# Kernel tuning notes

Hardware: AMD Instinct MI355X
Metric: run time of the kernel (lower is better)

## Reference

```python
import jax, jax.numpy as jnp
import numpy as np

HEADS = 8
DIM_HEAD = 64
SCALE = DIM_HEAD ** -0.5


def setup_inputs() -> dict:
    key = jax.random.key(0)
    ks = jax.random.split(key, 6)
    B, N, M = 4, 4096, 1024
    QD, CD, ID = 320, 768, 512
    s = lambda d: (1.0 / np.sqrt(d)).astype(np.float32)
    return {
        "x": jax.random.normal(ks[0], (B, N, QD), dtype=jnp.float32),
        "context": jax.random.normal(ks[1], (B, M, CD), dtype=jnp.float32),
        "Wq": jax.random.normal(ks[2], (QD, ID), dtype=jnp.float32) * s(QD),
        "Wk": jax.random.normal(ks[3], (CD, ID), dtype=jnp.float32) * s(CD),
        "Wv": jax.random.normal(ks[4], (CD, ID), dtype=jnp.float32) * s(CD),
        "Wo": jax.random.normal(ks[5], (ID, QD), dtype=jnp.float32) * s(ID),
        "bo": jnp.zeros((QD,), dtype=jnp.float32),
    }


def reference(x, context, Wq, Wk, Wv, Wo, bo):
    B, N, _ = x.shape
    M = context.shape[1]
    # projections
    q = (x @ Wq).reshape(B, N, HEADS, DIM_HEAD)        # b n h d
    k = (context @ Wk).reshape(B, M, HEADS, DIM_HEAD)  # b m h d
    v = (context @ Wv).reshape(B, M, HEADS, DIM_HEAD)
    # scaled dot-product attention per head
    scores = jnp.einsum("bnhd,bmhd->bhnm", q, k) * SCALE
    attn = jax.nn.softmax(scores, axis=-1)
    out = jnp.einsum("bhnm,bmhd->bnhd", attn, v).reshape(B, N, HEADS * DIM_HEAD)
    # output projection (dropout p=0.0 is identity)
    return out @ Wo + bo
```

## Files before the change

### kernel.cpp

```cpp
#include <hip/hip_runtime.h>
#include <cmath>

constexpr int BATCH  = 4;
constexpr int SEQ_N  = 4096;
constexpr int SEQ_M  = 1024;
constexpr int QD     = 320;
constexpr int CD     = 768;
constexpr int ID     = 512;
constexpr float QFOLD = 0.125f * 1.44269504f;
constexpr float EK2F  = -8.0f * 1.44269504f;

typedef __bf16 bf16x8 __attribute__((ext_vector_type(8)));
typedef __bf16 bf16x4 __attribute__((ext_vector_type(4)));
typedef __bf16 bf16x2 __attribute__((ext_vector_type(2)));
typedef float  f32x4  __attribute__((ext_vector_type(4)));

__device__ __forceinline__ void gload_lds16(const __bf16* g, __bf16* l) {
    __builtin_amdgcn_global_load_lds(
        (const __attribute__((address_space(1))) void*)g,
        (__attribute__((address_space(3))) void*)l, 16, 0, 0);
}

__device__ __forceinline__ float fast_exp2(float x) {
#if __has_builtin(__builtin_amdgcn_exp2f)
    return __builtin_amdgcn_exp2f(x);
#else
    return exp2f(x);
#endif
}

__global__ __launch_bounds__(256)
void cvt_all(const float* __restrict__ x, const float* __restrict__ ctx,
             const float* __restrict__ Wq, const float* __restrict__ Wk,
             const float* __restrict__ Wv, const float* __restrict__ Wo,
             __bf16* __restrict__ xb, __bf16* __restrict__ ctxb,
             __bf16* __restrict__ WqT, __bf16* __restrict__ WkT,
             __bf16* __restrict__ WvT, __bf16* __restrict__ WoT) {
    __shared__ float tile[32][33];
    int bid = blockIdx.x;
    if (bid < 4096) {
        constexpr int NX8 = SEQ_N * BATCH * QD / 8;
        int i = bid * 256 + threadIdx.x;
        const float* s; __bf16* d; int j;
        if (i < NX8) { s = x; d = xb; j = i; }
        else         { s = ctx; d = ctxb; j = i - NX8; }
        const float4* sp = reinterpret_cast<const float4*>(s) + (size_t)j * 2;
        float4 a = sp[0], b = sp[1];
        bf16x8 o = { (__bf16)a.x, (__bf16)a.y, (__bf16)a.z, (__bf16)a.w,
                     (__bf16)b.x, (__bf16)b.y, (__bf16)b.z, (__bf16)b.w };
        reinterpret_cast<bf16x8*>(d)[j] = o;
        return;
    }
    int wb = bid - 4096;
    const float* W; __bf16* WT; int K, N, tid; float scl = 1.0f;
    if (wb < 160)      { W = Wq; WT = WqT; K = 320; N = 512; tid = wb; scl = QFOLD; }
    else if (wb < 544) { W = Wk; WT = WkT; K = 768; N = 512; tid = wb - 160; }
    else if (wb < 928) { W = Wv; WT = WvT; K = 768; N = 512; tid = wb - 544; }
    else               { W = Wo; WT = WoT; K = 512; N = 320; tid = wb - 928; }
    int kt = K / 32;
    int k0 = (tid % kt) * 32, n0 = (tid / kt) * 32;
    int tc = threadIdx.x & 31, tr = threadIdx.x >> 5;
#pragma unroll
    for (int p = 0; p < 4; ++p)
        tile[p * 8 + tr][tc] = W[(size_t)(k0 + p * 8 + tr) * N + n0 + tc];
    __syncthreads();
#pragma unroll
    for (int p = 0; p < 4; ++p)
        WT[(size_t)(n0 + p * 8 + tr) * K + k0 + tc] = (__bf16)(tile[tc][p * 8 + tr] * scl);
}

__global__ __launch_bounds__(256)
void gemm_kv(const __bf16* __restrict__ A, const __bf16* __restrict__ BT,
             __bf16* __restrict__ Kb, __bf16* __restrict__ Vt, int M, int K) {
    __shared__ __attribute__((aligned(16))) __bf16 sA[2][128][64];
    __shared__ __attribute__((aligned(16))) __bf16 sB[2][64][64];

    const int t = threadIdx.x;
    const int wave = t >> 6, lane = t & 63;
    const int q = lane >> 4, c = lane & 15;
    const int wm = wave >> 1, wn = wave & 1;
    const int row0 = blockIdx.x * 128, col0 = blockIdx.y * 64;
    const int srow = lane >> 3, sch = lane & 7;
    const int fch = sch ^ srow;

    auto stage = [&](int buf, int k0) {
#pragma unroll
        for (int i = 0; i < 4; ++i) {
            int r = wave * 32 + i * 8;
            gload_lds16(A + (size_t)(row0 + r + srow) * K + k0 + fch * 8,
                        &sA[buf][r][0] + lane * 8);
        }
#pragma unroll
        for (int i = 0; i < 2; ++i) {
            int r = wave * 16 + i * 8;
            gload_lds16(BT + (size_t)(col0 + r + srow) * K + k0 + fch * 8,
                        &sB[buf][r][0] + lane * 8);
        }
    };

    f32x4 acc[4][2] = {};
    stage(0, 0);
    const int iters = K >> 6;
    for (int it = 0; it < iters; ++it) {
        const int p = it & 1;
        __syncthreads();
        if (it + 1 < iters) stage(p ^ 1, (it + 1) * 64);
#pragma unroll
        for (int ks = 0; ks < 2; ++ks) {
            const int so = ((ks * 4 + q) ^ (c & 7)) * 8;
            bf16x8 am[4], bn[2];
#pragma unroll
            for (int i = 0; i < 4; ++i)
                am[i] = *reinterpret_cast<const bf16x8*>(&sA[p][wm * 64 + i * 16 + c][0] + so);
#pragma unroll
            for (int j = 0; j < 2; ++j)
                bn[j] = *reinterpret_cast<const bf16x8*>(&sB[p][wn * 32 + j * 16 + c][0] + so);
#pragma unroll
            for (int i = 0; i < 4; ++i)
#pragma unroll
                for (int j = 0; j < 2; ++j)
                    acc[i][j] = __builtin_amdgcn_mfma_f32_16x16x32_bf16(bn[j], am[i], acc[i][j], 0, 0, 0);
        }
    }

    if (blockIdx.y < 8) {
#pragma unroll
        for (int i = 0; i < 4; ++i)
#pragma unroll
            for (int j = 0; j < 2; ++j) {
                int mrow = row0 + wm * 64 + i * 16 + c;
                int ncol = col0 + wn * 32 + j * 16 + q * 4;
                bf16x4 v = { (__bf16)acc[i][j][0], (__bf16)acc[i][j][1],
                             (__bf16)acc[i][j][2], (__bf16)acc[i][j][3] };
                *reinterpret_cast<bf16x4*>(&Kb[(size_t)mrow * 512 + ncol]) = v;
            }
    } else {
        __bf16* ldsT = (__bf16*)sA;
        __syncthreads();
#pragma unroll
        for (int i = 0; i < 4; ++i)
#pragma unroll
            for (int j = 0; j < 2; ++j) {
                int ml = wm * 64 + i * 16 + c;
                int dl = wn * 32 + j * 16 + q * 4;
#pragma unroll
                for (int r = 0; r < 4; ++r)
                    ldsT[(dl + r) * 136 + ml] = (__bf16)acc[i][j][r];
            }
        __syncthreads();
        int b = row0 >> 10, m0 = row0 & 1023;
        int h = (col0 - 512) >> 6;
        int d = t >> 2, ch = t & 3;
        __bf16* dst = Vt + (((size_t)((b * 8 + h) * 64 + d)) << 10) + m0 + ch * 32;
        const __bf16* src = &ldsT[d * 136 + ch * 32];
#pragma unroll
        for (int u = 0; u < 4; ++u)
            *reinterpret_cast<bf16x8*>(dst + u * 8) = *reinterpret_cast<const bf16x8*>(src + u * 8);
    }
}

__global__ __launch_bounds__(256, 2)
void flash_attn(const __bf16* __restrict__ xb, const __bf16* __restrict__ WqT,
                const __bf16* __restrict__ Kb, const __bf16* __restrict__ Vt,
                __bf16* __restrict__ AO) {
    __shared__ __attribute__((aligned(16))) __bf16 smem[20480];

    const int t = threadIdx.x;
    const int wave = t >> 6, lane = t & 63;
    const int q = lane >> 4, c = lane & 15;
    const int bh = blockIdx.y;
    const int b = bh >> 3, h = bh & 7;
    const int n0 = blockIdx.x * 256;
    const int srow = lane >> 3, sch = lane & 7;
    const int fch = sch ^ srow;

    f32x4 accQ[4][4] = {};
    {
        __bf16* sX = smem;
        __bf16* sW = smem + 16384;
        for (int k0 = 0; k0 < QD; k0 += 64) {
            __syncthreads();
#pragma unroll
            for (int i = 0; i < 8; ++i) {
                int r = wave * 64 + i * 8;
                gload_lds16(xb + (size_t)(b * SEQ_N + n0 + r + srow) * QD + k0 + fch * 8,
                            sX + r * 64 + lane * 8);
            }
#pragma unroll
            for (int i = 0; i < 2; ++i) {
                int r = wave * 16 + i * 8;
                gload_lds16(WqT + (size_t)(h * 64 + r + srow) * QD + k0 + fch * 8,
                            sW + r * 64 + lane * 8);
            }
            __syncthreads();
#pragma unroll
            for (int ks = 0; ks < 2; ++ks) {
                const int so = ((ks * 4 + q) ^ (c & 7)) * 8;
                bf16x8 aw[4], bx[4];
#pragma unroll
                for (int dt = 0; dt < 4; ++dt)
                    aw[dt] = *reinterpret_cast<const bf16x8*>(sW + (dt * 16 + c) * 64 + so);
#pragma unroll
                for (int qt = 0; qt < 4; ++qt)
                    bx[qt] = *reinterpret_cast<const bf16x8*>(sX + (wave * 64 + qt * 16 + c) * 64 + so);
#pragma unroll
                for (int dt = 0; dt < 4; ++dt)
#pragma unroll
                    for (int qt = 0; qt < 4; ++qt)
                        accQ[dt][qt] = __builtin_amdgcn_mfma_f32_16x16x32_bf16(aw[dt], bx[qt], accQ[dt][qt], 0, 0, 0);
            }
        }
    }
    __syncthreads();

    __bf16* sQw = smem + wave * 4608;
#pragma unroll
    for (int dt = 0; dt < 4; ++dt)
#pragma unroll
        for (int qt = 0; qt < 4; ++qt) {
            bf16x2 w0 = { (__bf16)accQ[dt][qt][0], (__bf16)accQ[dt][qt][1] };
            bf16x2 w1 = { (__bf16)accQ[dt][qt][2], (__bf16)accQ[dt][qt][3] };
            __bf16* pr = sQw + (qt * 16 + c) * 72 + dt * 16 + q * 4;
            *reinterpret_cast<bf16x2*>(pr)     = w0;
            *reinterpret_cast<bf16x2*>(pr + 2) = w1;
        }
    bf16x8 aq[4][2];
#pragma unroll
    for (int qt = 0; qt < 4; ++qt)
#pragma unroll
        for (int ks = 0; ks < 2; ++ks)
            aq[qt][ks] = *reinterpret_cast<const bf16x8*>(sQw + (qt * 16 + c) * 72 + ks * 32 + q * 8);
    __syncthreads();

    auto stageKV = [&](int buf, int m0) {
        __bf16* sK = smem + buf * 8192;
        __bf16* sV = smem + buf * 8192 + 4096;
#pragma unroll
        for (int i = 0; i < 2; ++i) {
            int r = wave * 16 + i * 8;
            int rho = r + srow;
            int kl = (rho & 32) | (((rho & 15) >> 2) << 3)
                   | (rho & 3) | (((rho >> 4) & 1) << 2);
            gload_lds16(Kb + (size_t)(b * SEQ_M + m0 + kl) * ID + h * 64 + fch * 8,
                        sK + r * 64 + lane * 8);
            gload_lds16(Vt + (((size_t)((b * 8 + h) * 64 + rho)) << 10) + m0 + fch * 8,
                        sV + r * 64 + lane * 8);
        }
    };

    const f32x4 ekc = { EK2F, EK2F, EK2F, EK2F };
    const bf16x8 ONES = { (__bf16)1.0f, (__bf16)1.0f, (__bf16)1.0f, (__bf16)1.0f,
                          (__bf16)1.0f, (__bf16)1.0f, (__bf16)1.0f, (__bf16)1.0f };
    f32x4 accO[4][4] = {};
    f32x4 accL[4] = {};

    stageKV(0, 0);
    constexpr int TILES = SEQ_M / 64;
    for (int mt = 0; mt < TILES; ++mt) {
        const int p = mt & 1;
        __syncthreads();
        if (mt + 1 < TILES) stageKV(p ^ 1, (mt + 1) * 64);
        const __bf16* sK = smem + p * 8192;
        const __bf16* sV = smem + p * 8192 + 4096;

        f32x4 s[4][4];
        __builtin_amdgcn_s_setprio(1);
#pragma unroll
        for (int ks = 0; ks < 2; ++ks) {
            const int so = ((ks * 4 + q) ^ (c & 7)) * 8;
#pragma unroll
            for (int ct = 0; ct < 4; ++ct) {
                bf16x8 ak = *reinterpret_cast<const bf16x8*>(sK + (ct * 16 + c) * 64 + so);
#pragma unroll
                for (int qt = 0; qt < 4; ++qt)
                    s[qt][ct] = (ks == 0)
                        ? __builtin_amdgcn_mfma_f32_16x16x32_bf16(ak, aq[qt][0], ekc, 0, 0, 0)
                        : __builtin_amdgcn_mfma_f32_16x16x32_bf16(ak, aq[qt][1], s[qt][ct], 0, 0, 0);
            }
        }
        __builtin_amdgcn_s_setprio(0);

        bf16x8 bp[4][2];
#pragma unroll
        for (int qt = 0; qt < 4; ++qt) {
            float pp[16];
#pragma unroll
            for (int ct = 0; ct < 4; ++ct)
#pragma unroll
                for (int r = 0; r < 4; ++r)
                    pp[ct * 4 + r] = fast_exp2(s[qt][ct][r]);
#pragma unroll
            for (int g = 0; g < 2; ++g)
                bp[qt][g] = bf16x8{ (__bf16)pp[g * 8 + 0], (__bf16)pp[g * 8 + 1],
                                    (__bf16)pp[g * 8 + 2], (__bf16)pp[g * 8 + 3],
                                    (__bf16)pp[g * 8 + 4], (__bf16)pp[g * 8 + 5],
                                    (__bf16)pp[g * 8 + 6], (__bf16)pp[g * 8 + 7] };
        }

        __builtin_amdgcn_s_setprio(1);
#pragma unroll
        for (int ks = 0; ks < 2; ++ks) {
            const int so = ((ks * 4 + q) ^ (c & 7)) * 8;
#pragma unroll
            for (int qt = 0; qt < 4; ++qt)
                accL[qt] = __builtin_amdgcn_mfma_f32_16x16x32_bf16(ONES, bp[qt][ks], accL[qt], 0, 0, 0);
#pragma unroll
            for (int nt = 0; nt < 4; ++nt) {
                bf16x8 av = *reinterpret_cast<const bf16x8*>(sV + (nt * 16 + c) * 64 + so);
#pragma unroll
                for (int qt = 0; qt < 4; ++qt)
                    accO[qt][nt] = __builtin_amdgcn_mfma_f32_16x16x32_bf16(av, bp[qt][ks], accO[qt][nt], 0, 0, 0);
            }
        }
        __builtin_amdgcn_s_setprio(0);
    }

#pragma unroll
    for (int qt = 0; qt < 4; ++qt) {
        float inv = 1.0f / accL[qt][0];
        size_t rowb = (size_t)(b * SEQ_N + n0 + wave * 64 + qt * 16 + c) * ID + h * 64;
#pragma unroll
        for (int nt = 0; nt < 4; ++nt) {
            bf16x4 v = { (__bf16)(accO[qt][nt][0] * inv), (__bf16)(accO[qt][nt][1] * inv),
                         (__bf16)(accO[qt][nt][2] * inv), (__bf16)(accO[qt][nt][3] * inv) };
            *reinterpret_cast<bf16x4*>(&AO[rowb + nt * 16 + q * 4]) = v;
        }
    }
}

__global__ __launch_bounds__(256)
void gemm_out(const __bf16* __restrict__ A, const __bf16* __restrict__ BT,
              const float* __restrict__ bias, float* __restrict__ C,
              int M, int N, int K) {
    __shared__ __attribute__((aligned(16))) __bf16 sA[2][128][64];
    __shared__ __attribute__((aligned(16))) __bf16 sB[2][64][64];

    const int t = threadIdx.x;
    const int wave = t >> 6, lane = t & 63;
    const int q = lane >> 4, c = lane & 15;
    const int wm = wave >> 1, wn = wave & 1;
    const int row0 = blockIdx.x * 128, col0 = blockIdx.y * 64;
    const int srow = lane >> 3, sch = lane & 7;
    const int fch = sch ^ srow;

    auto stage = [&](int buf, int k0) {
#pragma unroll
        for (int i = 0; i < 4; ++i) {
            int r = wave * 32 + i * 8;
            gload_lds16(A + (size_t)(row0 + r + srow) * K + k0 + fch * 8,
                        &sA[buf][r][0] + lane * 8);
        }
#pragma unroll
        for (int i = 0; i < 2; ++i) {
            int r = wave * 16 + i * 8;
            gload_lds16(BT + (size_t)(col0 + r + srow) * K + k0 + fch * 8,
                        &sB[buf][r][0] + lane * 8);
        }
    };

    f32x4 acc[4][2] = {};
    stage(0, 0);
    const int iters = K >> 6;
    for (int it = 0; it < iters; ++it) {
        const int p = it & 1;
        __syncthreads();
        if (it + 1 < iters) stage(p ^ 1, (it + 1) * 64);
#pragma unroll
        for (int ks = 0; ks < 2; ++ks) {
            const int so = ((ks * 4 + q) ^ (c & 7)) * 8;
            bf16x8 am[4], bn[2];
#pragma unroll
            for (int i = 0; i < 4; ++i)
                am[i] = *reinterpret_cast<const bf16x8*>(&sA[p][wm * 64 + i * 16 + c][0] + so);
#pragma unroll
            for (int j = 0; j < 2; ++j)
                bn[j] = *reinterpret_cast<const bf16x8*>(&sB[p][wn * 32 + j * 16 + c][0] + so);
#pragma unroll
            for (int i = 0; i < 4; ++i)
#pragma unroll
                for (int j = 0; j < 2; ++j)
                    acc[i][j] = __builtin_amdgcn_mfma_f32_16x16x32_bf16(bn[j], am[i], acc[i][j], 0, 0, 0);
        }
    }

#pragma unroll
    for (int i = 0; i < 4; ++i)
#pragma unroll
        for (int j = 0; j < 2; ++j) {
            int mrow = row0 + wm * 64 + i * 16 + c;
            int ncol = col0 + wn * 32 + j * 16 + q * 4;
            float4 v = { acc[i][j][0] + bias[ncol + 0],
                         acc[i][j][1] + bias[ncol + 1],
                         acc[i][j][2] + bias[ncol + 2],
                         acc[i][j][3] + bias[ncol + 3] };
            *reinterpret_cast<float4*>(&C[(size_t)mrow * N + ncol]) = v;
        }
}

extern "C" void kernel_launch(void* const* d_in, const int* in_sizes, int n_in,
                              void* d_out, int out_size, void* d_ws, size_t ws_size,
                              hipStream_t stream) {
    const float* x   = (const float*)d_in[0];
    const float* ctx = (const float*)d_in[1];
    const float* Wq  = (const float*)d_in[2];
    const float* Wk  = (const float*)d_in[3];
    const float* Wv  = (const float*)d_in[4];
    const float* Wo  = (const float*)d_in[5];
    const float* bo  = (const float*)d_in[6];
    float* out = (float*)d_out;

    char* ws = (char*)d_ws;
    __bf16* xb   = (__bf16*)(ws + 0);
    __bf16* ctxb = (__bf16*)(ws + 10485760);
    __bf16* AO   = (__bf16*)(ws + 16777216);
    __bf16* Kb   = (__bf16*)(ws + 33554432);
    __bf16* Vt   = (__bf16*)(ws + 37748736);
    __bf16* WqT  = (__bf16*)(ws + 41943040);
    __bf16* WkT  = (__bf16*)(ws + 42270720);
    __bf16* WvT  = (__bf16*)(ws + 43057152);
    __bf16* WoT  = (__bf16*)(ws + 43843584);

    const int MX = BATCH * SEQ_N;
    const int MC = BATCH * SEQ_M;
    dim3 blk(256);

    cvt_all<<<dim3(5184), blk, 0, stream>>>(x, ctx, Wq, Wk, Wv, Wo,
                                            xb, ctxb, WqT, WkT, WvT, WoT);

    gemm_kv<<<dim3(MC / 128, 16), blk, 0, stream>>>(ctxb, WkT, Kb, Vt, MC, CD);

    flash_attn<<<dim3(SEQ_N / 256, 32), blk, 0, stream>>>(xb, WqT, Kb, Vt, AO);

    gemm_out<<<dim3(MX / 128, QD / 64), blk, 0, stream>>>(AO, WoT, bo, out, MX, QD, ID);
}
```

Measured before the change: 155.5 us.

## Overlap x conversion with KV GEMM and software-pipeline two KV tiles per iteration

The fp32-to-bf16 conversion of x moves out of the pre-pass kernel and into extra blocks of the KV projection GEMM launch (now a 1D grid), so it runs alongside the GEMM instead of before it. In flash attention, each loop iteration now processes two 64-row K/V tiles and interleaves the second tile's QK MFMAs with the first tile's exp2 and PV, so MFMA and transcendental work can overlap. The s_setprio hints are dropped. LDS use grows from 40KB to 64KB per block for four tile buffers, which may limit the two-blocks-per-CU occupancy target, and the extra live score/probability registers raise register pressure.

```diff
diff --git a/kernel.cpp b/kernel.cpp
--- a/kernel.cpp
+++ b/kernel.cpp
@@ -30,33 +30,29 @@
 }
 
 __global__ __launch_bounds__(256)
-void cvt_all(const float* __restrict__ x, const float* __restrict__ ctx,
+void cvt_pre(const float* __restrict__ ctx,
              const float* __restrict__ Wq, const float* __restrict__ Wk,
              const float* __restrict__ Wv, const float* __restrict__ Wo,
-             __bf16* __restrict__ xb, __bf16* __restrict__ ctxb,
+             __bf16* __restrict__ ctxb,
              __bf16* __restrict__ WqT, __bf16* __restrict__ WkT,
              __bf16* __restrict__ WvT, __bf16* __restrict__ WoT) {
     __shared__ float tile[32][33];
     int bid = blockIdx.x;
-    if (bid < 4096) {
-        constexpr int NX8 = SEQ_N * BATCH * QD / 8;
-        int i = bid * 256 + threadIdx.x;
-        const float* s; __bf16* d; int j;
-        if (i < NX8) { s = x; d = xb; j = i; }
-        else         { s = ctx; d = ctxb; j = i - NX8; }
-        const float4* sp = reinterpret_cast<const float4*>(s) + (size_t)j * 2;
+    if (bid < 1536) {
+        int j = bid * 256 + threadIdx.x;
+        const float4* sp = reinterpret_cast<const float4*>(ctx) + (size_t)j * 2;
         float4 a = sp[0], b = sp[1];
         bf16x8 o = { (__bf16)a.x, (__bf16)a.y, (__bf16)a.z, (__bf16)a.w,
                      (__bf16)b.x, (__bf16)b.y, (__bf16)b.z, (__bf16)b.w };
-        reinterpret_cast<bf16x8*>(d)[j] = o;
+        reinterpret_cast<bf16x8*>(ctxb)[j] = o;
         return;
     }
-    int wb = bid - 4096;
+    int wb = bid - 1536;
     const float* W; __bf16* WT; int K, N, tid; float scl = 1.0f;
-    if (wb < 160)      { W = Wq; WT = WqT; K = 320; N = 512; tid = wb; scl = QFOLD; }
-    else if (wb < 544) { W = Wk; WT = WkT; K = 768; N = 512; tid = wb - 160; }
-    else if (wb < 928) { W = Wv; WT = WvT; K = 768; N = 512; tid = wb - 544; }
-    else               { W = Wo; WT = WoT; K = 512; N = 320; tid = wb - 928; }
+    if (wb < 384)       { W = Wk; WT = WkT; K = 768; N = 512; tid = wb; }
+    else if (wb < 768)  { W = Wv; WT = WvT; K = 768; N = 512; tid = wb - 384; }
+    else if (wb < 928)  { W = Wq; WT = WqT; K = 320; N = 512; tid = wb - 768; scl = QFOLD; }
+    else                { W = Wo; WT = WoT; K = 512; N = 320; tid = wb - 928; }
     int kt = K / 32;
     int k0 = (tid % kt) * 32, n0 = (tid / kt) * 32;
     int tc = threadIdx.x & 31, tr = threadIdx.x >> 5;
@@ -71,15 +67,28 @@
 
 __global__ __launch_bounds__(256)
 void gemm_kv(const __bf16* __restrict__ A, const __bf16* __restrict__ BT,
-             __bf16* __restrict__ Kb, __bf16* __restrict__ Vt, int M, int K) {
+             const float* __restrict__ x, __bf16* __restrict__ Kb,
+             __bf16* __restrict__ Vt, __bf16* __restrict__ xb, int K) {
     __shared__ __attribute__((aligned(16))) __bf16 sA[2][128][64];
     __shared__ __attribute__((aligned(16))) __bf16 sB[2][64][64];
+
+    int bid = blockIdx.x;
+    if (bid >= 512) {
+        int j = (bid - 512) * 256 + threadIdx.x;
+        const float4* sp = reinterpret_cast<const float4*>(x) + (size_t)j * 2;
+        float4 a = sp[0], b = sp[1];
+        bf16x8 o = { (__bf16)a.x, (__bf16)a.y, (__bf16)a.z, (__bf16)a.w,
+                     (__bf16)b.x, (__bf16)b.y, (__bf16)b.z, (__bf16)b.w };
+        reinterpret_cast<bf16x8*>(xb)[j] = o;
+        return;
+    }
 
     const int t = threadIdx.x;
     const int wave = t >> 6, lane = t & 63;
     const int q = lane >> 4, c = lane & 15;
     const int wm = wave >> 1, wn = wave & 1;
-    const int row0 = blockIdx.x * 128, col0 = blockIdx.y * 64;
+    const int by = bid >> 5;
+    const int row0 = (bid & 31) * 128, col0 = by * 64;
     const int srow = lane >> 3, sch = lane & 7;
     const int fch = sch ^ srow;
 
@@ -123,7 +132,7 @@
         }
     }
 
-    if (blockIdx.y < 8) {
+    if (by < 8) {
 #pragma unroll
         for (int i = 0; i < 4; ++i)
 #pragma unroll
@@ -163,7 +172,7 @@
 void flash_attn(const __bf16* __restrict__ xb, const __bf16* __restrict__ WqT,
                 const __bf16* __restrict__ Kb, const __bf16* __restrict__ Vt,
                 __bf16* __restrict__ AO) {
-    __shared__ __attribute__((aligned(16))) __bf16 smem[20480];
+    __shared__ __attribute__((aligned(16))) __bf16 smem[32768];
 
     const int t = threadIdx.x;
     const int wave = t >> 6, lane = t & 63;
@@ -232,9 +241,9 @@
             aq[qt][ks] = *reinterpret_cast<const bf16x8*>(sQw + (qt * 16 + c) * 72 + ks * 32 + q * 8);
     __syncthreads();
 
-    auto stageKV = [&](int buf, int m0) {
-        __bf16* sK = smem + buf * 8192;
-        __bf16* sV = smem + buf * 8192 + 4096;
+    auto stageT = [&](int ts, int m0) {
+        __bf16* sK = smem + ts * 8192;
+        __bf16* sV = smem + ts * 8192 + 4096;
 #pragma unroll
         for (int i = 0; i < 2; ++i) {
             int r = wave * 16 + i * 8;
@@ -254,17 +263,7 @@
     f32x4 accO[4][4] = {};
     f32x4 accL[4] = {};
 
-    stageKV(0, 0);
-    constexpr int TILES = SEQ_M / 64;
-    for (int mt = 0; mt < TILES; ++mt) {
-        const int p = mt & 1;
-        __syncthreads();
-        if (mt + 1 < TILES) stageKV(p ^ 1, (mt + 1) * 64);
-        const __bf16* sK = smem + p * 8192;
-        const __bf16* sV = smem + p * 8192 + 4096;
-
-        f32x4 s[4][4];
-        __builtin_amdgcn_s_setprio(1);
+    auto QK = [&](const __bf16* sK, f32x4 (&sarr)[4][4]) {
 #pragma unroll
         for (int ks = 0; ks < 2; ++ks) {
             const int so = ((ks * 4 + q) ^ (c & 7)) * 8;
@@ -273,14 +272,13 @@
                 bf16x8 ak = *reinterpret_cast<const bf16x8*>(sK + (ct * 16 + c) * 64 + so);
 #pragma unroll
                 for (int qt = 0; qt < 4; ++qt)
-                    s[qt][ct] = (ks == 0)
+                    sarr[qt][ct] = (ks == 0)
                         ? __builtin_amdgcn_mfma_f32_16x16x32_bf16(ak, aq[qt][0], ekc, 0, 0, 0)
-                        : __builtin_amdgcn_mfma_f32_16x16x32_bf16(ak, aq[qt][1], s[qt][ct], 0, 0, 0);
-            }
-        }
-        __builtin_amdgcn_s_setprio(0);
-
-        bf16x8 bp[4][2];
+                        : __builtin_amdgcn_mfma_f32_16x16x32_bf16(ak, aq[qt][1], sarr[qt][ct], 0, 0, 0);
+            }
+        }
+    };
+    auto EXP2P = [&](const f32x4 (&sarr)[4][4], bf16x8 (&bp)[4][2]) {
 #pragma unroll
         for (int qt = 0; qt < 4; ++qt) {
             float pp[16];
@@ -288,7 +286,7 @@
             for (int ct = 0; ct < 4; ++ct)
 #pragma unroll
                 for (int r = 0; r < 4; ++r)
-                    pp[ct * 4 + r] = fast_exp2(s[qt][ct][r]);
+                    pp[ct * 4 + r] = fast_exp2(sarr[qt][ct][r]);
 #pragma unroll
             for (int g = 0; g < 2; ++g)
                 bp[qt][g] = bf16x8{ (__bf16)pp[g * 8 + 0], (__bf16)pp[g * 8 + 1],
@@ -296,8 +294,8 @@
                                     (__bf16)pp[g * 8 + 4], (__bf16)pp[g * 8 + 5],
                                     (__bf16)pp[g * 8 + 6], (__bf16)pp[g * 8 + 7] };
         }
-
-        __builtin_amdgcn_s_setprio(1);
+    };
+    auto PV = [&](const __bf16* sV, const bf16x8 (&bp)[4][2]) {
 #pragma unroll
         for (int ks = 0; ks < 2; ++ks) {
             const int so = ((ks * 4 + q) ^ (c & 7)) * 8;
@@ -312,7 +310,31 @@
                     accO[qt][nt] = __builtin_amdgcn_mfma_f32_16x16x32_bf16(av, bp[qt][ks], accO[qt][nt], 0, 0, 0);
             }
         }
-        __builtin_amdgcn_s_setprio(0);
+    };
+
+    stageT(0, 0);
+    stageT(1, 64);
+    constexpr int ITERS = SEQ_M / 128;
+    for (int it = 0; it < ITERS; ++it) {
+        const int p = it & 1;
+        __syncthreads();
+        if (it + 1 < ITERS) {
+            stageT((p ^ 1) * 2,     (2 * it + 2) * 64);
+            stageT((p ^ 1) * 2 + 1, (2 * it + 3) * 64);
+        }
+        const __bf16* sKA = smem + (2 * p) * 8192;
+        const __bf16* sVA = sKA + 4096;
+        const __bf16* sKB = smem + (2 * p + 1) * 8192;
+        const __bf16* sVB = sKB + 4096;
+
+        f32x4 sA_[4][4]; bf16x8 bpA[4][2];
+        QK(sKA, sA_);
+        EXP2P(sA_, bpA);
+        f32x4 sB_[4][4]; bf16x8 bpB[4][2];
+        QK(sKB, sB_);
+        PV(sVA, bpA);
+        EXP2P(sB_, bpB);
+        PV(sVB, bpB);
     }
 
 #pragma unroll
@@ -421,13 +443,12 @@
     __bf16* WoT  = (__bf16*)(ws + 43843584);
 
     const int MX = BATCH * SEQ_N;
-    const int MC = BATCH * SEQ_M;
     dim3 blk(256);
 
-    cvt_all<<<dim3(5184), blk, 0, stream>>>(x, ctx, Wq, Wk, Wv, Wo,
-                                            xb, ctxb, WqT, WkT, WvT, WoT);
-
-    gemm_kv<<<dim3(MC / 128, 16), blk, 0, stream>>>(ctxb, WkT, Kb, Vt, MC, CD);
+    cvt_pre<<<dim3(2624), blk, 0, stream>>>(ctx, Wq, Wk, Wv, Wo,
+                                            ctxb, WqT, WkT, WvT, WoT);
+
+    gemm_kv<<<dim3(3072), blk, 0, stream>>>(ctxb, WkT, x, Kb, Vt, xb, CD);
 
     flash_attn<<<dim3(SEQ_N / 256, 32), blk, 0, stream>>>(xb, WqT, Kb, Vt, AO);
 
```

Result: slower. 170.9 us (+9.9%).

## Stagger wave groups so half the waves run PV while others run QK

Applied to the files above, without the earlier changes.

The flash-attention loop now splits the four waves into two groups. One group runs QK, exp and PV on the current tile. The other group defers PV of the previous tile to the start of the next iteration, so matrix-core work and exp work from different waves interleave. The K/V LDS ring grows from two to four slots so the deferred group can still read the previous V tile. This raises LDS use to 64KB per block, which may limit occupancy at two blocks per CU, and it removes the setprio hints.

```diff
diff --git a/kernel.cpp b/kernel.cpp
--- a/kernel.cpp
+++ b/kernel.cpp
@@ -163,7 +163,7 @@
 void flash_attn(const __bf16* __restrict__ xb, const __bf16* __restrict__ WqT,
                 const __bf16* __restrict__ Kb, const __bf16* __restrict__ Vt,
                 __bf16* __restrict__ AO) {
-    __shared__ __attribute__((aligned(16))) __bf16 smem[20480];
+    __shared__ __attribute__((aligned(16))) __bf16 smem[32768];
 
     const int t = threadIdx.x;
     const int wave = t >> 6, lane = t & 63;
@@ -232,9 +232,9 @@
             aq[qt][ks] = *reinterpret_cast<const bf16x8*>(sQw + (qt * 16 + c) * 72 + ks * 32 + q * 8);
     __syncthreads();
 
-    auto stageKV = [&](int buf, int m0) {
-        __bf16* sK = smem + buf * 8192;
-        __bf16* sV = smem + buf * 8192 + 4096;
+    auto stageKV = [&](int slot, int m0) {
+        __bf16* sK = smem + slot * 8192;
+        __bf16* sV = smem + slot * 8192 + 4096;
 #pragma unroll
         for (int i = 0; i < 2; ++i) {
             int r = wave * 16 + i * 8;
@@ -254,17 +254,7 @@
     f32x4 accO[4][4] = {};
     f32x4 accL[4] = {};
 
-    stageKV(0, 0);
-    constexpr int TILES = SEQ_M / 64;
-    for (int mt = 0; mt < TILES; ++mt) {
-        const int p = mt & 1;
-        __syncthreads();
-        if (mt + 1 < TILES) stageKV(p ^ 1, (mt + 1) * 64);
-        const __bf16* sK = smem + p * 8192;
-        const __bf16* sV = smem + p * 8192 + 4096;
-
-        f32x4 s[4][4];
-        __builtin_amdgcn_s_setprio(1);
+    auto QK = [&](const __bf16* sK, f32x4 (&sarr)[4][4]) {
 #pragma unroll
         for (int ks = 0; ks < 2; ++ks) {
             const int so = ((ks * 4 + q) ^ (c & 7)) * 8;
@@ -273,14 +263,13 @@
                 bf16x8 ak = *reinterpret_cast<const bf16x8*>(sK + (ct * 16 + c) * 64 + so);
 #pragma unroll
                 for (int qt = 0; qt < 4; ++qt)
-                    s[qt][ct] = (ks == 0)
+                    sarr[qt][ct] = (ks == 0)
                         ? __builtin_amdgcn_mfma_f32_16x16x32_bf16(ak, aq[qt][0], ekc, 0, 0, 0)
-                        : __builtin_amdgcn_mfma_f32_16x16x32_bf16(ak, aq[qt][1], s[qt][ct], 0, 0, 0);
-            }
-        }
-        __builtin_amdgcn_s_setprio(0);
-
-        bf16x8 bp[4][2];
+                        : __builtin_amdgcn_mfma_f32_16x16x32_bf16(ak, aq[qt][1], sarr[qt][ct], 0, 0, 0);
+            }
+        }
+    };
+    auto EXP2P = [&](const f32x4 (&sarr)[4][4], bf16x8 (&bp)[4][2]) {
 #pragma unroll
         for (int qt = 0; qt < 4; ++qt) {
             float pp[16];
@@ -288,7 +277,7 @@
             for (int ct = 0; ct < 4; ++ct)
 #pragma unroll
                 for (int r = 0; r < 4; ++r)
-                    pp[ct * 4 + r] = fast_exp2(s[qt][ct][r]);
+                    pp[ct * 4 + r] = fast_exp2(sarr[qt][ct][r]);
 #pragma unroll
             for (int g = 0; g < 2; ++g)
                 bp[qt][g] = bf16x8{ (__bf16)pp[g * 8 + 0], (__bf16)pp[g * 8 + 1],
@@ -296,8 +285,8 @@
                                     (__bf16)pp[g * 8 + 4], (__bf16)pp[g * 8 + 5],
                                     (__bf16)pp[g * 8 + 6], (__bf16)pp[g * 8 + 7] };
         }
-
-        __builtin_amdgcn_s_setprio(1);
+    };
+    auto PV = [&](const __bf16* sV, const bf16x8 (&bp)[4][2]) {
 #pragma unroll
         for (int ks = 0; ks < 2; ++ks) {
             const int so = ((ks * 4 + q) ^ (c & 7)) * 8;
@@ -312,8 +301,31 @@
                     accO[qt][nt] = __builtin_amdgcn_mfma_f32_16x16x32_bf16(av, bp[qt][ks], accO[qt][nt], 0, 0, 0);
             }
         }
-        __builtin_amdgcn_s_setprio(0);
-    }
+    };
+
+    stageKV(0, 0);
+    f32x4 s[4][4];
+    bf16x8 bp[4][2];
+    const bool gA = (wave < 2);
+    constexpr int TILES = SEQ_M / 64;
+    for (int mt = 0; mt < TILES; ++mt) {
+        __syncthreads();
+        if (mt + 1 < TILES) stageKV((mt + 1) & 3, (mt + 1) * 64);
+        const __bf16* sK  = smem + (mt & 3) * 8192;
+        const __bf16* sV  = sK + 4096;
+        const __bf16* sVp = smem + ((mt - 1) & 3) * 8192 + 4096;
+
+        if (gA) {
+            QK(sK, s);
+            EXP2P(s, bp);
+            PV(sV, bp);
+        } else {
+            if (mt > 0) PV(sVp, bp);
+            QK(sK, s);
+            EXP2P(s, bp);
+        }
+    }
+    if (!gA) PV(smem + ((TILES - 1) & 3) * 8192 + 4096, bp);
 
 #pragma unroll
     for (int qt = 0; qt < 4; ++qt) {
```

After: 157.6 us. No clear change (+1.4%).

## Fuse fp32-to-bf16 conversion of x into attention Q projection, VALU row sums

Applied to the files above, without the earlier changes.

Removes the separate conversion pass of x to bf16. The attention kernel now loads fp32 x directly from global memory and converts it to bf16 in registers before writing to LDS, which saves a full write and re-read of the xb buffer. The softmax denominator is now accumulated with VALU adds and finished with cross-lane shuffles instead of extra MFMAs against a ones vector. The setprio hints are also dropped. In exchange, each x tile is now loaded 8 times (once per head block), reading fp32 instead of bf16 and going through registers instead of direct-to-LDS loads.

```diff
diff --git a/kernel.cpp b/kernel.cpp
--- a/kernel.cpp
+++ b/kernel.cpp
@@ -30,33 +30,29 @@
 }
 
 __global__ __launch_bounds__(256)
-void cvt_all(const float* __restrict__ x, const float* __restrict__ ctx,
+void cvt_pre(const float* __restrict__ ctx,
              const float* __restrict__ Wq, const float* __restrict__ Wk,
              const float* __restrict__ Wv, const float* __restrict__ Wo,
-             __bf16* __restrict__ xb, __bf16* __restrict__ ctxb,
+             __bf16* __restrict__ ctxb,
              __bf16* __restrict__ WqT, __bf16* __restrict__ WkT,
              __bf16* __restrict__ WvT, __bf16* __restrict__ WoT) {
     __shared__ float tile[32][33];
     int bid = blockIdx.x;
-    if (bid < 4096) {
-        constexpr int NX8 = SEQ_N * BATCH * QD / 8;
-        int i = bid * 256 + threadIdx.x;
-        const float* s; __bf16* d; int j;
-        if (i < NX8) { s = x; d = xb; j = i; }
-        else         { s = ctx; d = ctxb; j = i - NX8; }
-        const float4* sp = reinterpret_cast<const float4*>(s) + (size_t)j * 2;
+    if (bid < 1536) {
+        int j = bid * 256 + threadIdx.x;
+        const float4* sp = reinterpret_cast<const float4*>(ctx) + (size_t)j * 2;
         float4 a = sp[0], b = sp[1];
         bf16x8 o = { (__bf16)a.x, (__bf16)a.y, (__bf16)a.z, (__bf16)a.w,
                      (__bf16)b.x, (__bf16)b.y, (__bf16)b.z, (__bf16)b.w };
-        reinterpret_cast<bf16x8*>(d)[j] = o;
+        reinterpret_cast<bf16x8*>(ctxb)[j] = o;
         return;
     }
-    int wb = bid - 4096;
+    int wb = bid - 1536;
     const float* W; __bf16* WT; int K, N, tid; float scl = 1.0f;
-    if (wb < 160)      { W = Wq; WT = WqT; K = 320; N = 512; tid = wb; scl = QFOLD; }
-    else if (wb < 544) { W = Wk; WT = WkT; K = 768; N = 512; tid = wb - 160; }
-    else if (wb < 928) { W = Wv; WT = WvT; K = 768; N = 512; tid = wb - 544; }
-    else               { W = Wo; WT = WoT; K = 512; N = 320; tid = wb - 928; }
+    if (wb < 384)       { W = Wk; WT = WkT; K = 768; N = 512; tid = wb; }
+    else if (wb < 768)  { W = Wv; WT = WvT; K = 768; N = 512; tid = wb - 384; }
+    else if (wb < 928)  { W = Wq; WT = WqT; K = 320; N = 512; tid = wb - 768; scl = QFOLD; }
+    else                { W = Wo; WT = WoT; K = 512; N = 320; tid = wb - 928; }
     int kt = K / 32;
     int k0 = (tid % kt) * 32, n0 = (tid / kt) * 32;
     int tc = threadIdx.x & 31, tr = threadIdx.x >> 5;
@@ -160,7 +156,7 @@
 }
 
 __global__ __launch_bounds__(256, 2)
-void flash_attn(const __bf16* __restrict__ xb, const __bf16* __restrict__ WqT,
+void flash_attn(const float* __restrict__ x, const __bf16* __restrict__ WqT,
                 const __bf16* __restrict__ Kb, const __bf16* __restrict__ Vt,
                 __bf16* __restrict__ AO) {
     __shared__ __attribute__((aligned(16))) __bf16 smem[20480];
@@ -179,12 +175,23 @@
         __bf16* sX = smem;
         __bf16* sW = smem + 16384;
         for (int k0 = 0; k0 < QD; k0 += 64) {
-            __syncthreads();
+            f32x4 xr[8][2];
 #pragma unroll
             for (int i = 0; i < 8; ++i) {
                 int r = wave * 64 + i * 8;
-                gload_lds16(xb + (size_t)(b * SEQ_N + n0 + r + srow) * QD + k0 + fch * 8,
-                            sX + r * 64 + lane * 8);
+                const float* gp = x + (size_t)(b * SEQ_N + n0 + r + srow) * QD + k0 + fch * 8;
+                xr[i][0] = *reinterpret_cast<const f32x4*>(gp);
+                xr[i][1] = *reinterpret_cast<const f32x4*>(gp + 4);
+            }
+            __syncthreads();
+#pragma unroll
+            for (int i = 0; i < 8; ++i) {
+                int r = wave * 64 + i * 8;
+                bf16x8 o = { (__bf16)xr[i][0][0], (__bf16)xr[i][0][1],
+                             (__bf16)xr[i][0][2], (__bf16)xr[i][0][3],
+                             (__bf16)xr[i][1][0], (__bf16)xr[i][1][1],
+                             (__bf16)xr[i][1][2], (__bf16)xr[i][1][3] };
+                *reinterpret_cast<bf16x8*>(sX + r * 64 + lane * 8) = o;
             }
 #pragma unroll
             for (int i = 0; i < 2; ++i) {
@@ -249,10 +256,8 @@
     };
 
     const f32x4 ekc = { EK2F, EK2F, EK2F, EK2F };
-    const bf16x8 ONES = { (__bf16)1.0f, (__bf16)1.0f, (__bf16)1.0f, (__bf16)1.0f,
-                          (__bf16)1.0f, (__bf16)1.0f, (__bf16)1.0f, (__bf16)1.0f };
     f32x4 accO[4][4] = {};
-    f32x4 accL[4] = {};
+    float psum[4] = {};
 
     stageKV(0, 0);
     constexpr int TILES = SEQ_M / 64;
@@ -264,7 +269,6 @@
         const __bf16* sV = smem + p * 8192 + 4096;
 
         f32x4 s[4][4];
-        __builtin_amdgcn_s_setprio(1);
 #pragma unroll
         for (int ks = 0; ks < 2; ++ks) {
             const int so = ((ks * 4 + q) ^ (c & 7)) * 8;
@@ -278,7 +282,6 @@
                         : __builtin_amdgcn_mfma_f32_16x16x32_bf16(ak, aq[qt][1], s[qt][ct], 0, 0, 0);
             }
         }
-        __builtin_amdgcn_s_setprio(0);
 
         bf16x8 bp[4][2];
 #pragma unroll
@@ -295,16 +298,16 @@
                                     (__bf16)pp[g * 8 + 2], (__bf16)pp[g * 8 + 3],
                                     (__bf16)pp[g * 8 + 4], (__bf16)pp[g * 8 + 5],
                                     (__bf16)pp[g * 8 + 6], (__bf16)pp[g * 8 + 7] };
-        }
-
-        __builtin_amdgcn_s_setprio(1);
+            psum[qt] += (((pp[0] + pp[1]) + (pp[2] + pp[3])) +
+                         ((pp[4] + pp[5]) + (pp[6] + pp[7]))) +
+                        (((pp[8] + pp[9]) + (pp[10] + pp[11])) +
+                         ((pp[12] + pp[13]) + (pp[14] + pp[15])));
+        }
+
 #pragma unroll
         for (int ks = 0; ks < 2; ++ks) {
             const int so = ((ks * 4 + q) ^ (c & 7)) * 8;
 #pragma unroll
-            for (int qt = 0; qt < 4; ++qt)
-                accL[qt] = __builtin_amdgcn_mfma_f32_16x16x32_bf16(ONES, bp[qt][ks], accL[qt], 0, 0, 0);
-#pragma unroll
             for (int nt = 0; nt < 4; ++nt) {
                 bf16x8 av = *reinterpret_cast<const bf16x8*>(sV + (nt * 16 + c) * 64 + so);
 #pragma unroll
@@ -312,12 +315,14 @@
                     accO[qt][nt] = __builtin_amdgcn_mfma_f32_16x16x32_bf16(av, bp[qt][ks], accO[qt][nt], 0, 0, 0);
             }
         }
-        __builtin_amdgcn_s_setprio(0);
     }
 
 #pragma unroll
     for (int qt = 0; qt < 4; ++qt) {
-        float inv = 1.0f / accL[qt][0];
+        float l = psum[qt];
+        l += __shfl_xor(l, 16);
+        l += __shfl_xor(l, 32);
+        float inv = 1.0f / l;
         size_t rowb = (size_t)(b * SEQ_N + n0 + wave * 64 + qt * 16 + c) * ID + h * 64;
 #pragma unroll
         for (int nt = 0; nt < 4; ++nt) {
@@ -410,7 +415,6 @@
     float* out = (float*)d_out;
 
     char* ws = (char*)d_ws;
-    __bf16* xb   = (__bf16*)(ws + 0);
     __bf16* ctxb = (__bf16*)(ws + 10485760);
     __bf16* AO   = (__bf16*)(ws + 16777216);
     __bf16* Kb   = (__bf16*)(ws + 33554432);
@@ -424,12 +428,12 @@
     const int MC = BATCH * SEQ_M;
     dim3 blk(256);
 
-    cvt_all<<<dim3(5184), blk, 0, stream>>>(x, ctx, Wq, Wk, Wv, Wo,
-                                            xb, ctxb, WqT, WkT, WvT, WoT);
+    cvt_pre<<<dim3(2624), blk, 0, stream>>>(ctx, Wq, Wk, Wv, Wo,
+                                            ctxb, WqT, WkT, WvT, WoT);
 
     gemm_kv<<<dim3(MC / 128, 16), blk, 0, stream>>>(ctxb, WkT, Kb, Vt, MC, CD);
 
-    flash_attn<<<dim3(SEQ_N / 256, 32), blk, 0, stream>>>(xb, WqT, Kb, Vt, AO);
+    flash_attn<<<dim3(SEQ_N / 256, 32), blk, 0, stream>>>(x, WqT, Kb, Vt, AO);
 
     gemm_out<<<dim3(MX / 128, QD / 64), blk, 0, stream>>>(AO, WoT, bo, out, MX, QD, ID);
 }
```

After: 158.7 us. 1.02x slower.
